# Kernel optimization log

Hardware: AMD Instinct MI355X
Metric: run time of the kernel (lower is better)

Reference implementation:

```python
import jax, jax.numpy as jnp
import numpy as np

HEAD_DIM = 256
N_Q = 8
N_KV = 4
HIDDEN = 2304
WINDOW = 1024
SOFT_CAP = 50.0
MAX_WAVELENGTH = 10000.0


def _rope(x, start_index=0):
    # x: [b, s, n, h]. keras_hub RotaryEmbedding (rotate-half convention),
    # followed by Gemma's interleave permutation of the feature dim.
    b, s, n, h = x.shape
    inv_freq = 1.0 / (MAX_WAVELENGTH ** (jnp.arange(0, h, 2, dtype=jnp.float32) / h))
    pos = jnp.arange(s, dtype=jnp.float32) + start_index
    freq = pos[:, None] * inv_freq[None, :]            # [s, h/2]
    emb = jnp.concatenate([freq, freq], axis=-1)[None, :, None, :]  # [1, s, 1, h]
    cos, sin = jnp.cos(emb).astype(x.dtype), jnp.sin(emb).astype(x.dtype)
    x1, x2 = jnp.split(x, 2, axis=-1)
    rot = jnp.concatenate([-x2, x1], axis=-1)
    y = x * cos + rot * sin
    # Gemma _apply_rope: split halves then interleave (same permutation on q and k)
    a, b2 = jnp.split(y, 2, axis=-1)
    return jnp.stack([a, b2], axis=-1).reshape(x.shape)


def setup_inputs() -> dict:
    key = jax.random.key(0)
    ks = jax.random.split(key, 5)
    B, T, D = 2, 2048, HIDDEN
    x = jax.random.normal(ks[0], (B, T, D), dtype=jnp.float32)
    # causal mask [b, q_len, kv_len]
    causal = jnp.tril(jnp.ones((T, T), dtype=bool))
    attention_mask = jnp.broadcast_to(causal[None], (B, T, T))
    scale = 0.02
    Wq = jax.random.normal(ks[1], (N_Q, D, HEAD_DIM), dtype=jnp.float32) * scale
    Wk = jax.random.normal(ks[2], (N_KV, D, HEAD_DIM), dtype=jnp.float32) * scale
    Wv = jax.random.normal(ks[3], (N_KV, D, HEAD_DIM), dtype=jnp.float32) * scale
    Wo = jax.random.normal(ks[4], (N_Q, HEAD_DIM, D), dtype=jnp.float32) * scale
    return {"x": x, "attention_mask": attention_mask, "Wq": Wq, "Wk": Wk, "Wv": Wv, "Wo": Wo}


def reference(x, attention_mask, Wq, Wk, Wv, Wo):
    b, t, d = x.shape
    q = jnp.einsum('btd,ndh->btnh', x, Wq)
    k = jnp.einsum('bsd,kdh->bskh', x, Wk)
    v = jnp.einsum('bsd,kdh->bskh', x, Wv)
    q = _rope(q)
    k = _rope(k)
    s = k.shape[1]
    # sliding window band mask (triu(-w+1) & tril(w-1)), rows sliced at cache_update_index=0
    i = jnp.arange(s)[:, None]
    j = jnp.arange(s)[None, :]
    sliding = (j - i <= WINDOW - 1) & (i - j <= WINDOW - 1)
    mask = attention_mask & sliding[None, :t, :s]      # [b, t, s]
    q = q * jnp.asarray(1.0 / np.sqrt(HEAD_DIM), dtype=q.dtype)
    g = N_Q // N_KV
    qg = q.reshape(b, t, N_KV, g, HEAD_DIM)
    logits = jnp.einsum('btkgh,bskh->bkgts', qg, k).astype(jnp.float32)
    logits = jnp.tanh(logits / SOFT_CAP) * SOFT_CAP    # logit soft-cap
    m = mask[:, None, None, :, :]                      # [b, 1, 1, t, s]
    logits = jnp.where(m, logits, jnp.float32(-1e30))
    probs = jax.nn.softmax(logits, axis=-1).astype(q.dtype)
    out = jnp.einsum('bkgts,bskh->btkgh', probs, v).reshape(b, t, N_Q, HEAD_DIM)
    no_attended = jnp.all(~attention_mask, axis=-1, keepdims=True)[..., None]  # [b, t, 1, 1]
    out = jnp.where(no_attended, jnp.zeros_like(out), out)
    return jnp.einsum('btnh,nhd->btd', out, Wo)
```

## Files before the change

### kernel.cpp

```cpp
#include <hip/hip_runtime.h>
#include <math.h>

#define HEAD_DIM 256
#define N_Q 8
#define N_KV 4
#define HIDDEN 2304
#define WINDOW 1024
#define BATCH 2
#define SEQ 2048
#define BT (BATCH*SEQ)

typedef unsigned short u16;
typedef __attribute__((ext_vector_type(8))) short bf16x8;
typedef __attribute__((ext_vector_type(4))) float f32x4;

__device__ __forceinline__ u16 f2bf(float f) {
    union { float f; unsigned u; } c; c.f = f;
    unsigned r = c.u + 0x7FFF + ((c.u >> 16) & 1);
    return (u16)(r >> 16);
}
__device__ __forceinline__ float bf2f(u16 b) {
    union { float f; unsigned u; } c; c.u = ((unsigned)b) << 16;
    return c.f;
}

__global__ __launch_bounds__(256) void convert_x_kernel(
    const float* __restrict__ x, u16* __restrict__ xb, int n8)
{
    int i = blockIdx.x * 256 + threadIdx.x;
    if (i >= n8) return;
    const float4 a = ((const float4*)x)[2*i];
    const float4 b = ((const float4*)x)[2*i+1];
    u16 o[8] = { f2bf(a.x), f2bf(a.y), f2bf(a.z), f2bf(a.w),
                 f2bf(b.x), f2bf(b.y), f2bf(b.z), f2bf(b.w) };
    ((uint4*)xb)[i] = *(const uint4*)o;
}

__global__ __launch_bounds__(256) void wqkv_t_kernel(
    const float* __restrict__ Wq, const float* __restrict__ Wk,
    const float* __restrict__ Wv, u16* __restrict__ Wt)
{
    __shared__ float t[32][33];
    const int j = blockIdx.z;
    const float* W = (j < 8)  ? Wq + (size_t)j*HIDDEN*HEAD_DIM
                   : (j < 12) ? Wk + (size_t)(j-8)*HIDDEN*HEAD_DIM
                              : Wv + (size_t)(j-12)*HIDDEN*HEAD_DIM;
    const int d0 = blockIdx.x * 32, h0 = blockIdx.y * 32;
    const int tx = threadIdx.x & 31, ty = threadIdx.x >> 5;
    #pragma unroll
    for (int i = 0; i < 4; i++)
        t[ty + i*8][tx] = W[(size_t)(d0 + ty + i*8)*HEAD_DIM + h0 + tx];
    __syncthreads();
    #pragma unroll
    for (int i = 0; i < 4; i++)
        Wt[(size_t)(j*256 + h0 + ty + i*8)*HIDDEN + d0 + tx] = f2bf(t[tx][ty + i*8]);
}

__global__ __launch_bounds__(256) void wo_t_kernel(
    const float* __restrict__ Wo, u16* __restrict__ Wot)
{
    __shared__ float t[32][33];
    const int k0 = blockIdx.x * 32, d0 = blockIdx.y * 32;
    const int tx = threadIdx.x & 31, ty = threadIdx.x >> 5;
    #pragma unroll
    for (int i = 0; i < 4; i++)
        t[ty + i*8][tx] = Wo[(size_t)(k0 + ty + i*8)*HIDDEN + d0 + tx];
    __syncthreads();
    #pragma unroll
    for (int i = 0; i < 4; i++)
        Wot[(size_t)(d0 + ty + i*8)*(N_Q*HEAD_DIM) + k0 + tx] = f2bf(t[tx][ty + i*8]);
}

template<typename OutT>
__global__ __launch_bounds__(256) void gemm_bf16_kernel(
    const u16* __restrict__ A, const u16* __restrict__ Bt,
    OutT* __restrict__ C, int M, int N, int K)
{
    __shared__ u16 As[128*32];
    __shared__ u16 Bs[128*32];
    const int m0 = blockIdx.y * 128;
    const int n0 = blockIdx.x * 128;
    const int tid  = threadIdx.x;
    const int lane = tid & 63;
    const int wave = tid >> 6;
    const int wm = (wave & 1) * 64;
    const int wn = (wave >> 1) * 64;
    const int l16  = lane & 15;
    const int quad = lane >> 4;

    const int srow = wave*16 + (lane >> 2);
    const int sseg = lane & 3;
    const u16* Ag = A  + (size_t)(m0 + srow)*K + sseg*8;
    const u16* Bg = Bt + (size_t)(n0 + srow)*K + sseg*8;

    const u16* ArA = As + (wm + l16)*32 + quad*8;
    const u16* BrB = Bs + (wn + l16)*32 + quad*8;

    f32x4 acc[4][4];
    #pragma unroll
    for (int i = 0; i < 4; i++)
        #pragma unroll
        for (int j = 0; j < 4; j++) acc[i][j] = (f32x4){0.f,0.f,0.f,0.f};

    for (int k0 = 0; k0 < K; k0 += 32) {
        __syncthreads();
        #pragma unroll
        for (int c = 0; c < 2; c++) {
            __builtin_amdgcn_global_load_lds(
                (const __attribute__((address_space(1))) unsigned int*)(Ag + (size_t)c*64*K + k0),
                (__attribute__((address_space(3))) unsigned int*)&As[(c*64 + wave*16)*32],
                16, 0, 0);
            __builtin_amdgcn_global_load_lds(
                (const __attribute__((address_space(1))) unsigned int*)(Bg + (size_t)c*64*K + k0),
                (__attribute__((address_space(3))) unsigned int*)&Bs[(c*64 + wave*16)*32],
                16, 0, 0);
        }
        __syncthreads();
        bf16x8 af[4], bfr[4];
        #pragma unroll
        for (int t = 0; t < 4; t++) af[t]  = *(const bf16x8*)(ArA + t*16*32);
        #pragma unroll
        for (int t = 0; t < 4; t++) bfr[t] = *(const bf16x8*)(BrB + t*16*32);
        #pragma unroll
        for (int i = 0; i < 4; i++)
            #pragma unroll
            for (int j = 0; j < 4; j++)
                acc[i][j] = __builtin_amdgcn_mfma_f32_16x16x32_bf16(
                                af[i], bfr[j], acc[i][j], 0, 0, 0);
    }

    #pragma unroll
    for (int i = 0; i < 4; i++) {
        const int rbase = m0 + wm + i*16 + quad*4;
        #pragma unroll
        for (int j = 0; j < 4; j++) {
            const int col = n0 + wn + j*16 + l16;
            #pragma unroll
            for (int r = 0; r < 4; r++) {
                const float v = acc[i][j][r];
                if constexpr (sizeof(OutT) == 2)
                    ((u16*)C)[(size_t)(rbase + r)*N + col] = f2bf(v);
                else
                    ((float*)C)[(size_t)(rbase + r)*N + col] = v;
            }
        }
    }
}

__global__ __launch_bounds__(256) void rope_kernel(
    const u16* __restrict__ raw, u16* __restrict__ qb, u16* __restrict__ kbf)
{
    const int r   = blockIdx.x;
    const int pos = r & (SEQ-1);
    const int tid = threadIdx.x;
    const u16* row = raw + (size_t)r * 4096;
    const float LOG1E4 = 9.210340371976184f;

    #pragma unroll
    for (int p = tid; p < 1024; p += 256) {
        const int n = p >> 7, j = p & 127;
        const float lo = bf2f(row[n*256 + j]);
        const float hi = bf2f(row[n*256 + j + 128]);
        const float inv = __expf(-LOG1E4 * (float)j * (1.0f/128.0f));
        float s, c; sincosf((float)pos * inv, &s, &c);
        qb[((size_t)r*N_Q + n)*HEAD_DIM + j]       = f2bf((lo*c - hi*s) * 0.0625f);
        qb[((size_t)r*N_Q + n)*HEAD_DIM + j + 128] = f2bf((hi*c + lo*s) * 0.0625f);
    }
    #pragma unroll
    for (int p = tid; p < 512; p += 256) {
        const int n = p >> 7, j = p & 127;
        const float lo = bf2f(row[2048 + n*256 + j]);
        const float hi = bf2f(row[2048 + n*256 + j + 128]);
        const float inv = __expf(-LOG1E4 * (float)j * (1.0f/128.0f));
        float s, c; sincosf((float)pos * inv, &s, &c);
        kbf[((size_t)r*N_KV + n)*HEAD_DIM + j]       = f2bf(lo*c - hi*s);
        kbf[((size_t)r*N_KV + n)*HEAD_DIM + j + 128] = f2bf(hi*c + lo*s);
    }
}

__global__ __launch_bounds__(256) void vtrans_kernel(
    const u16* __restrict__ raw, u16* __restrict__ vtt)
{
    __shared__ u16 T[32*264];
    const int blk = blockIdx.x;
    const int sc  = blk & 63;
    const int bk  = blk >> 6;
    const int b   = bk >> 2, kh = bk & 3;
    const int tid = threadIdx.x;

    const u16* rrow = raw + (size_t)(b*SEQ + sc*32)*4096 + 3072 + kh*256;
    {
        const int s = tid >> 3;
        #pragma unroll
        for (int it = 0; it < 4; it++) {
            const int seg = (tid & 7) + it*8;
            *(uint4*)&T[s*264 + seg*8] = *(const uint4*)(rrow + (size_t)s*4096 + seg*8);
        }
    }
    __syncthreads();
    u16* out = vtt + (size_t)blk*8192;
    #pragma unroll
    for (int it = 0; it < 4; it++) {
        const int o = tid + it*256;
        const int h = o >> 2, ss = o & 3;
        u16 tmp[8];
        #pragma unroll
        for (int j = 0; j < 8; j++) tmp[j] = T[(ss*8 + j)*264 + h];
        *(uint4*)(out + h*32 + ss*8) = *(const uint4*)tmp;
    }
}

#define AQT 64
__global__ __launch_bounds__(256) void attn_mfma_kernel(
    const u16* __restrict__ qb, const u16* __restrict__ kb,
    const u16* __restrict__ vtt, u16* __restrict__ ao)
{
    __shared__ u16 Ks[32*264];
    __shared__ u16 Vs[256*40];
    __shared__ u16 Ps[64*40];

    const int qh = blockIdx.y;
    const int kh = qh >> 1;
    const int t0 = blockIdx.x * AQT;
    const int b  = t0 >> 11;
    const int tb = t0 & (SEQ-1);
    const int tid  = threadIdx.x;
    const int wave = tid >> 6;
    const int lane = tid & 63;
    const int l16  = lane & 15;
    const int quad = lane >> 4;

    bf16x8 qf[8];
    {
        const u16* qrow = qb + ((size_t)(t0 + wave*16 + l16)*N_Q + qh)*HEAD_DIM + quad*8;
        #pragma unroll
        for (int c = 0; c < 8; c++) qf[c] = *(const bf16x8*)(qrow + c*32);
    }

    f32x4 o[16];
    #pragma unroll
    for (int n = 0; n < 16; n++) o[n] = (f32x4){0.f,0.f,0.f,0.f};
    float lpart[4] = {0.f, 0.f, 0.f, 0.f};

    int s_begin = tb - (WINDOW-1); if (s_begin < 0) s_begin = 0;
    const int st0 = s_begin & ~31;

    const u16* kbase = kb  + ((size_t)(b*SEQ)*N_KV + kh)*HEAD_DIM;
    const u16* vbase = vtt + ((size_t)(b*N_KV + kh)*SEQ)*HEAD_DIM;

    for (int st = st0; st < tb + AQT; st += 32) {
        __syncthreads();
        {
            const int s = tid >> 3;
            const u16* krow = kbase + (size_t)(st + s)*(N_KV*HEAD_DIM);
            #pragma unroll
            for (int it = 0; it < 4; it++) {
                const int seg = (tid & 7) + it*8;
                *(uint4*)&Ks[s*264 + seg*8] = *(const uint4*)(krow + seg*8);
            }
            const u16* vtile = vbase + (size_t)st*HEAD_DIM;
            #pragma unroll
            for (int it = 0; it < 4; it++) {
                const int idx = tid + it*256;
                const int h = idx >> 2, ss = idx & 3;
                *(uint4*)&Vs[h*40 + ss*8] = *(const uint4*)(vtile + h*32 + ss*8);
            }
        }
        __syncthreads();

        f32x4 sc[2];
        #pragma unroll
        for (int sf = 0; sf < 2; sf++) {
            f32x4 a = (f32x4){0.f,0.f,0.f,0.f};
            const u16* kr = &Ks[(sf*16 + l16)*264 + quad*8];
            #pragma unroll
            for (int c = 0; c < 8; c++)
                a = __builtin_amdgcn_mfma_f32_16x16x32_bf16(
                        qf[c], *(const bf16x8*)(kr + c*32), a, 0, 0, 0);
            sc[sf] = a;
        }

        #pragma unroll
        for (int sf = 0; sf < 2; sf++) {
            const int sg = st + sf*16 + l16;
            #pragma unroll
            for (int r = 0; r < 4; r++) {
                const int tg = tb + wave*16 + quad*4 + r;
                const float e1 = __expf(sc[sf][r] * 0.04f);
                float p = __expf(-100.0f / (e1 + 1.0f));
                const bool ok = (sg <= tg) && (tg - sg < WINDOW);
                p = ok ? p : 0.0f;
                lpart[r] += p;
                Ps[(wave*16 + quad*4 + r)*40 + sf*16 + l16] = f2bf(p);
            }
        }

        const bf16x8 ap = *(const bf16x8*)&Ps[(wave*16 + l16)*40 + quad*8];
        #pragma unroll
        for (int n = 0; n < 16; n++) {
            const bf16x8 bv = *(const bf16x8*)&Vs[(n*16 + l16)*40 + quad*8];
            o[n] = __builtin_amdgcn_mfma_f32_16x16x32_bf16(ap, bv, o[n], 0, 0, 0);
        }
    }

    float inv[4];
    #pragma unroll
    for (int r = 0; r < 4; r++) {
        float s = lpart[r];
        #pragma unroll
        for (int sh = 1; sh <= 8; sh <<= 1) s += __shfl_xor(s, sh, 64);
        inv[r] = 1.0f / (s + 1e-30f);
    }

    #pragma unroll
    for (int r = 0; r < 4; r++) {
        const int row = t0 + wave*16 + quad*4 + r;
        u16* arow = ao + ((size_t)row*N_Q + qh)*HEAD_DIM + l16;
        #pragma unroll
        for (int n = 0; n < 16; n++)
            arow[n*16] = f2bf(o[n][r] * inv[r]);
    }
}

extern "C" void kernel_launch(void* const* d_in, const int* in_sizes, int n_in,
                              void* d_out, int out_size, void* d_ws, size_t ws_size,
                              hipStream_t stream)
{
    const float* x  = (const float*)d_in[0];
    const float* Wq = (const float*)d_in[2];
    const float* Wk = (const float*)d_in[3];
    const float* Wv = (const float*)d_in[4];
    const float* Wo = (const float*)d_in[5];
    float* out = (float*)d_out;

    char* w = (char*)d_ws;
    u16* qbuf = (u16*)(w);
    u16* kbuf = (u16*)(w +  16777216ull);
    u16* vtt  = (u16*)(w +  25165824ull);
    u16* aob  = (u16*)(w +  33554432ull);
    u16* xb   = (u16*)(w +  50331648ull);
    u16* wt1  = (u16*)(w +  69206016ull);
    u16* wot  = (u16*)(w +  88080384ull);
    u16* raw  = (u16*)(w +  97517568ull);

    const int n8 = BT*HIDDEN/8;
    convert_x_kernel<<<(n8+255)/256, 256, 0, stream>>>(x, xb, n8);
    wqkv_t_kernel<<<dim3(HIDDEN/32, HEAD_DIM/32, 16), 256, 0, stream>>>(Wq, Wk, Wv, wt1);
    wo_t_kernel<<<dim3(N_Q*HEAD_DIM/32, HIDDEN/32), 256, 0, stream>>>(Wo, wot);

    gemm_bf16_kernel<u16><<<dim3(4096/128, BT/128), 256, 0, stream>>>(
        xb, wt1, raw, BT, 4096, HIDDEN);
    rope_kernel<<<BT, 256, 0, stream>>>(raw, qbuf, kbuf);
    vtrans_kernel<<<BATCH*N_KV*64, 256, 0, stream>>>(raw, vtt);
    attn_mfma_kernel<<<dim3(BT/AQT, N_Q), 256, 0, stream>>>(qbuf, kbuf, vtt, aob);
    gemm_bf16_kernel<float><<<dim3(HIDDEN/128, BT/128), 256, 0, stream>>>(
        aob, wot, out, BT, HIDDEN, N_Q*HEAD_DIM);
}
```

Baseline: 431.4 us.

## Widen GEMM K-tile with XOR swizzle, re-split attention PV work, vectorize transposes

The GEMM now stages 64-wide K tiles with an XOR-swizzled LDS layout, which halves the number of barrier pairs and is meant to avoid bank conflicts. The weight transpose kernels use 64x64 tiles with float4 loads and 16-byte bf16 stores. In attention, V tiles are pre-swizzled and loaded straight into LDS with global_load_lds. The PV product is re-split so each wave owns a 64-wide slice of the head dim across all 64 query rows, and half the heads walk query blocks in reverse to balance load. This adds an extra barrier per tile and an LDS row-sum exchange.

```diff
diff --git a/kernel.cpp b/kernel.cpp
--- a/kernel.cpp
+++ b/kernel.cpp
@@ -40,35 +40,63 @@
     const float* __restrict__ Wq, const float* __restrict__ Wk,
     const float* __restrict__ Wv, u16* __restrict__ Wt)
 {
-    __shared__ float t[32][33];
+    __shared__ float t[64][65];
     const int j = blockIdx.z;
     const float* W = (j < 8)  ? Wq + (size_t)j*HIDDEN*HEAD_DIM
                    : (j < 12) ? Wk + (size_t)(j-8)*HIDDEN*HEAD_DIM
                               : Wv + (size_t)(j-12)*HIDDEN*HEAD_DIM;
-    const int d0 = blockIdx.x * 32, h0 = blockIdx.y * 32;
-    const int tx = threadIdx.x & 31, ty = threadIdx.x >> 5;
-    #pragma unroll
-    for (int i = 0; i < 4; i++)
-        t[ty + i*8][tx] = W[(size_t)(d0 + ty + i*8)*HEAD_DIM + h0 + tx];
+    const int d0 = blockIdx.x * 64, h0 = blockIdx.y * 64;
+    const int tid = threadIdx.x;
+    {
+        const int r = tid >> 4, c4 = tid & 15;
+        #pragma unroll
+        for (int rr = r; rr < 64; rr += 16) {
+            const float4 v = *(const float4*)(W + (size_t)(d0+rr)*HEAD_DIM + h0 + c4*4);
+            t[rr][c4*4+0] = v.x; t[rr][c4*4+1] = v.y;
+            t[rr][c4*4+2] = v.z; t[rr][c4*4+3] = v.w;
+        }
+    }
     __syncthreads();
-    #pragma unroll
-    for (int i = 0; i < 4; i++)
-        Wt[(size_t)(j*256 + h0 + ty + i*8)*HIDDEN + d0 + tx] = f2bf(t[tx][ty + i*8]);
+    {
+        const int hh = tid >> 2;
+        #pragma unroll
+        for (int it = 0; it < 2; it++) {
+            const int chunk = (tid & 3) + it*4;
+            u16 tmp[8];
+            #pragma unroll
+            for (int jj = 0; jj < 8; jj++) tmp[jj] = f2bf(t[chunk*8+jj][hh]);
+            *(uint4*)&Wt[(size_t)(j*256 + h0 + hh)*HIDDEN + d0 + chunk*8] = *(const uint4*)tmp;
+        }
+    }
 }
 
 __global__ __launch_bounds__(256) void wo_t_kernel(
     const float* __restrict__ Wo, u16* __restrict__ Wot)
 {
-    __shared__ float t[32][33];
-    const int k0 = blockIdx.x * 32, d0 = blockIdx.y * 32;
-    const int tx = threadIdx.x & 31, ty = threadIdx.x >> 5;
-    #pragma unroll
-    for (int i = 0; i < 4; i++)
-        t[ty + i*8][tx] = Wo[(size_t)(k0 + ty + i*8)*HIDDEN + d0 + tx];
+    __shared__ float t[64][65];
+    const int k0 = blockIdx.x * 64, d0 = blockIdx.y * 64;
+    const int tid = threadIdx.x;
+    {
+        const int r = tid >> 4, c4 = tid & 15;
+        #pragma unroll
+        for (int rr = r; rr < 64; rr += 16) {
+            const float4 v = *(const float4*)(Wo + (size_t)(k0+rr)*HIDDEN + d0 + c4*4);
+            t[rr][c4*4+0] = v.x; t[rr][c4*4+1] = v.y;
+            t[rr][c4*4+2] = v.z; t[rr][c4*4+3] = v.w;
+        }
+    }
     __syncthreads();
-    #pragma unroll
-    for (int i = 0; i < 4; i++)
-        Wot[(size_t)(d0 + ty + i*8)*(N_Q*HEAD_DIM) + k0 + tx] = f2bf(t[tx][ty + i*8]);
+    {
+        const int dd = tid >> 2;
+        #pragma unroll
+        for (int it = 0; it < 2; it++) {
+            const int chunk = (tid & 3) + it*4;
+            u16 tmp[8];
+            #pragma unroll
+            for (int jj = 0; jj < 8; jj++) tmp[jj] = f2bf(t[chunk*8+jj][dd]);
+            *(uint4*)&Wot[(size_t)(d0 + dd)*(N_Q*HEAD_DIM) + k0 + chunk*8] = *(const uint4*)tmp;
+        }
+    }
 }
 
 template<typename OutT>
@@ -76,8 +104,8 @@
     const u16* __restrict__ A, const u16* __restrict__ Bt,
     OutT* __restrict__ C, int M, int N, int K)
 {
-    __shared__ u16 As[128*32];
-    __shared__ u16 Bs[128*32];
+    __shared__ u16 As[128*64];
+    __shared__ u16 Bs[128*64];
     const int m0 = blockIdx.y * 128;
     const int n0 = blockIdx.x * 128;
     const int tid  = threadIdx.x;
@@ -88,13 +116,14 @@
     const int l16  = lane & 15;
     const int quad = lane >> 4;
 
-    const int srow = wave*16 + (lane >> 2);
-    const int sseg = lane & 3;
-    const u16* Ag = A  + (size_t)(m0 + srow)*K + sseg*8;
-    const u16* Bg = Bt + (size_t)(n0 + srow)*K + sseg*8;
-
-    const u16* ArA = As + (wm + l16)*32 + quad*8;
-    const u16* BrB = Bs + (wn + l16)*32 + quad*8;
+    const int srow8  = lane >> 3;
+    const int schunk = (lane & 7) ^ srow8;
+    const u16* Ag = A  + (size_t)(m0 + wave*8 + srow8)*K + schunk*8;
+    const u16* Bg = Bt + (size_t)(n0 + wave*8 + srow8)*K + schunk*8;
+
+    const int axor = l16 & 7;
+    const u16* ArA = As + (wm + l16)*64;
+    const u16* BrB = Bs + (wn + l16)*64;
 
     f32x4 acc[4][4];
     #pragma unroll
@@ -102,31 +131,36 @@
         #pragma unroll
         for (int j = 0; j < 4; j++) acc[i][j] = (f32x4){0.f,0.f,0.f,0.f};
 
-    for (int k0 = 0; k0 < K; k0 += 32) {
+    for (int k0 = 0; k0 < K; k0 += 64) {
         __syncthreads();
         #pragma unroll
-        for (int c = 0; c < 2; c++) {
+        for (int c = 0; c < 4; c++) {
             __builtin_amdgcn_global_load_lds(
-                (const __attribute__((address_space(1))) unsigned int*)(Ag + (size_t)c*64*K + k0),
-                (__attribute__((address_space(3))) unsigned int*)&As[(c*64 + wave*16)*32],
+                (const __attribute__((address_space(1))) unsigned int*)(Ag + (size_t)c*32*K + k0),
+                (__attribute__((address_space(3))) unsigned int*)&As[(c*32 + wave*8)*64],
                 16, 0, 0);
             __builtin_amdgcn_global_load_lds(
-                (const __attribute__((address_space(1))) unsigned int*)(Bg + (size_t)c*64*K + k0),
-                (__attribute__((address_space(3))) unsigned int*)&Bs[(c*64 + wave*16)*32],
+                (const __attribute__((address_space(1))) unsigned int*)(Bg + (size_t)c*32*K + k0),
+                (__attribute__((address_space(3))) unsigned int*)&Bs[(c*32 + wave*8)*64],
                 16, 0, 0);
         }
         __syncthreads();
-        bf16x8 af[4], bfr[4];
-        #pragma unroll
-        for (int t = 0; t < 4; t++) af[t]  = *(const bf16x8*)(ArA + t*16*32);
-        #pragma unroll
-        for (int t = 0; t < 4; t++) bfr[t] = *(const bf16x8*)(BrB + t*16*32);
-        #pragma unroll
-        for (int i = 0; i < 4; i++)
-            #pragma unroll
-            for (int j = 0; j < 4; j++)
-                acc[i][j] = __builtin_amdgcn_mfma_f32_16x16x32_bf16(
-                                af[i], bfr[j], acc[i][j], 0, 0, 0);
+        #pragma unroll
+        for (int kk = 0; kk < 2; kk++) {
+            bf16x8 af[4], bfr[4];
+            #pragma unroll
+            for (int t = 0; t < 4; t++)
+                af[t]  = *(const bf16x8*)(ArA + t*16*64 + (((kk<<2)|quad) ^ axor)*8);
+            #pragma unroll
+            for (int t = 0; t < 4; t++)
+                bfr[t] = *(const bf16x8*)(BrB + t*16*64 + (((kk<<2)|quad) ^ axor)*8);
+            #pragma unroll
+            for (int i = 0; i < 4; i++)
+                #pragma unroll
+                for (int j = 0; j < 4; j++)
+                    acc[i][j] = __builtin_amdgcn_mfma_f32_16x16x32_bf16(
+                                    af[i], bfr[j], acc[i][j], 0, 0, 0);
+        }
     }
 
     #pragma unroll
@@ -206,7 +240,7 @@
         u16 tmp[8];
         #pragma unroll
         for (int j = 0; j < 8; j++) tmp[j] = T[(ss*8 + j)*264 + h];
-        *(uint4*)(out + h*32 + ss*8) = *(const uint4*)tmp;
+        *(uint4*)(out + h*32 + ((ss ^ (h & 3))*8)) = *(const uint4*)tmp;
     }
 }
 
@@ -216,12 +250,15 @@
     const u16* __restrict__ vtt, u16* __restrict__ ao)
 {
     __shared__ u16 Ks[32*264];
-    __shared__ u16 Vs[256*40];
+    __shared__ u16 Vs[256*32];
     __shared__ u16 Ps[64*40];
+    __shared__ float lsum[64];
 
     const int qh = blockIdx.y;
     const int kh = qh >> 1;
-    const int t0 = blockIdx.x * AQT;
+    const int bx = ((blockIdx.y >> 2) & 1) ? (gridDim.x - 1 - (int)blockIdx.x)
+                                           : (int)blockIdx.x;
+    const int t0 = bx * AQT;
     const int b  = t0 >> 11;
     const int tb = t0 & (SEQ-1);
     const int tid  = threadIdx.x;
@@ -237,9 +274,11 @@
         for (int c = 0; c < 8; c++) qf[c] = *(const bf16x8*)(qrow + c*32);
     }
 
-    f32x4 o[16];
-    #pragma unroll
-    for (int n = 0; n < 16; n++) o[n] = (f32x4){0.f,0.f,0.f,0.f};
+    f32x4 o[4][4];
+    #pragma unroll
+    for (int i = 0; i < 4; i++)
+        #pragma unroll
+        for (int j = 0; j < 4; j++) o[i][j] = (f32x4){0.f,0.f,0.f,0.f};
     float lpart[4] = {0.f, 0.f, 0.f, 0.f};
 
     int s_begin = tb - (WINDOW-1); if (s_begin < 0) s_begin = 0;
@@ -251,19 +290,21 @@
     for (int st = st0; st < tb + AQT; st += 32) {
         __syncthreads();
         {
+            const u16* vtile = vbase + (size_t)st*HEAD_DIM;
+            #pragma unroll
+            for (int c = 0; c < 4; c++) {
+                const int off = wave*2048 + c*512;
+                __builtin_amdgcn_global_load_lds(
+                    (const __attribute__((address_space(1))) unsigned int*)(vtile + off + lane*8),
+                    (__attribute__((address_space(3))) unsigned int*)&Vs[off],
+                    16, 0, 0);
+            }
             const int s = tid >> 3;
             const u16* krow = kbase + (size_t)(st + s)*(N_KV*HEAD_DIM);
             #pragma unroll
             for (int it = 0; it < 4; it++) {
                 const int seg = (tid & 7) + it*8;
                 *(uint4*)&Ks[s*264 + seg*8] = *(const uint4*)(krow + seg*8);
-            }
-            const u16* vtile = vbase + (size_t)st*HEAD_DIM;
-            #pragma unroll
-            for (int it = 0; it < 4; it++) {
-                const int idx = tid + it*256;
-                const int h = idx >> 2, ss = idx & 3;
-                *(uint4*)&Vs[h*40 + ss*8] = *(const uint4*)(vtile + h*32 + ss*8);
             }
         }
         __syncthreads();
@@ -294,31 +335,42 @@
                 Ps[(wave*16 + quad*4 + r)*40 + sf*16 + l16] = f2bf(p);
             }
         }
-
-        const bf16x8 ap = *(const bf16x8*)&Ps[(wave*16 + l16)*40 + quad*8];
-        #pragma unroll
-        for (int n = 0; n < 16; n++) {
-            const bf16x8 bv = *(const bf16x8*)&Vs[(n*16 + l16)*40 + quad*8];
-            o[n] = __builtin_amdgcn_mfma_f32_16x16x32_bf16(ap, bv, o[n], 0, 0, 0);
-        }
-    }
-
-    float inv[4];
+        __syncthreads();
+
+        bf16x8 ap[4];
+        #pragma unroll
+        for (int i = 0; i < 4; i++)
+            ap[i] = *(const bf16x8*)&Ps[(i*16 + l16)*40 + quad*8];
+        #pragma unroll
+        for (int j = 0; j < 4; j++) {
+            const int hr = wave*64 + j*16 + l16;
+            const bf16x8 bv = *(const bf16x8*)&Vs[hr*32 + ((quad ^ (l16 & 3))*8)];
+            #pragma unroll
+            for (int i = 0; i < 4; i++)
+                o[i][j] = __builtin_amdgcn_mfma_f32_16x16x32_bf16(ap[i], bv, o[i][j], 0, 0, 0);
+        }
+    }
+
     #pragma unroll
     for (int r = 0; r < 4; r++) {
         float s = lpart[r];
         #pragma unroll
         for (int sh = 1; sh <= 8; sh <<= 1) s += __shfl_xor(s, sh, 64);
-        inv[r] = 1.0f / (s + 1e-30f);
-    }
-
-    #pragma unroll
-    for (int r = 0; r < 4; r++) {
-        const int row = t0 + wave*16 + quad*4 + r;
-        u16* arow = ao + ((size_t)row*N_Q + qh)*HEAD_DIM + l16;
-        #pragma unroll
-        for (int n = 0; n < 16; n++)
-            arow[n*16] = f2bf(o[n][r] * inv[r]);
+        if (l16 == 0) lsum[wave*16 + quad*4 + r] = s;
+    }
+    __syncthreads();
+
+    #pragma unroll
+    for (int i = 0; i < 4; i++) {
+        #pragma unroll
+        for (int r = 0; r < 4; r++) {
+            const int rl  = i*16 + quad*4 + r;
+            const float inv = 1.0f / (lsum[rl] + 1e-30f);
+            u16* arow = ao + ((size_t)(t0 + rl)*N_Q + qh)*HEAD_DIM + wave*64 + l16;
+            #pragma unroll
+            for (int j = 0; j < 4; j++)
+                arow[j*16] = f2bf(o[i][j][r] * inv);
+        }
     }
 }
 
@@ -345,8 +397,8 @@
 
     const int n8 = BT*HIDDEN/8;
     convert_x_kernel<<<(n8+255)/256, 256, 0, stream>>>(x, xb, n8);
-    wqkv_t_kernel<<<dim3(HIDDEN/32, HEAD_DIM/32, 16), 256, 0, stream>>>(Wq, Wk, Wv, wt1);
-    wo_t_kernel<<<dim3(N_Q*HEAD_DIM/32, HIDDEN/32), 256, 0, stream>>>(Wo, wot);
+    wqkv_t_kernel<<<dim3(HIDDEN/64, HEAD_DIM/64, 16), 256, 0, stream>>>(Wq, Wk, Wv, wt1);
+    wo_t_kernel<<<dim3(N_Q*HEAD_DIM/64, HIDDEN/64), 256, 0, stream>>>(Wo, wot);
 
     gemm_bf16_kernel<u16><<<dim3(4096/128, BT/128), 256, 0, stream>>>(
         xb, wt1, raw, BT, 4096, HIDDEN);
```

Measured after the change: 415.4 us. 1.04x faster.
